# Optimization experiments

Measured on AMD Instinct MI355X. Metric: run time of the kernel, lower is better.

## Reference

```python
import jax, jax.numpy as jnp
import numpy as np

N = 50000          # nodes
E = 400000         # edges
MUL0 = 16          # multiplicity of 0e irreps (node & message)
MUL1 = 8           # multiplicity of 1o irreps
RBF = 8
HID = 64
CUTOFF = 5.0
WNUM = MUL0*MUL0 + MUL1*MUL0 + MUL0*MUL1 + MUL1*MUL1  # 576 tp weights per edge
EPS = 1e-8
INV_SQRT3 = 1.0 / np.sqrt(3.0).astype(np.float32)
A_PATH = 1.0 / np.sqrt(float(MUL0 + MUL1))  # e3nn path normalization (fan_in = 24 for both outputs)


def _split_sv(x):
    # x: [n, 40] -> scalars [n,16], vectors [n,8,3]
    return x[:, :MUL0], x[:, MUL0:].reshape(-1, MUL1, 3)


def _irrep_norm(x):
    # RMS-normalize each irrep block separately (IrrepNorm)
    s, v = _split_sv(x)
    s_rms = jnp.sqrt(jnp.mean(s * s, axis=-1, keepdims=True) + EPS)
    v_rms = jnp.sqrt(jnp.mean(jnp.sum(v * v, axis=-1), axis=-1, keepdims=True) + EPS)
    return jnp.concatenate([s / s_rms, (v / v_rms[:, :, None]).reshape(-1, MUL1 * 3)], axis=-1)


def setup_inputs() -> dict:
    key = jax.random.key(0)
    ks = jax.random.split(key, 20)
    inp = {
        'x': jax.random.normal(ks[0], (N, MUL0 + 3 * MUL1), jnp.float32),
        'edge_src': jax.random.randint(ks[1], (E,), 0, N, jnp.int32),
        'edge_dst': jax.random.randint(ks[2], (E,), 0, N, jnp.int32),
        'edge_sh': jax.random.normal(ks[3], (E, 4), jnp.float32),
        'edge_rbf': jax.random.uniform(ks[4], (E, RBF), jnp.float32),
        'edge_len': jax.random.uniform(ks[5], (E,), jnp.float32) * CUTOFF,
        # radial MLP producing per-edge TP weights
        'w_r1': jax.random.normal(ks[6], (RBF, HID), jnp.float32) / np.sqrt(RBF),
        'b_r1': jnp.zeros((HID,), jnp.float32),
        'w_r2': jax.random.normal(ks[7], (HID, WNUM), jnp.float32) / np.sqrt(HID),
        'b_r2': jnp.zeros((WNUM,), jnp.float32),
        # edge gate MLP
        'w_g1': jax.random.normal(ks[8], (RBF, HID), jnp.float32) / np.sqrt(RBF),
        'b_g1': jnp.zeros((HID,), jnp.float32),
        'w_g2': jax.random.normal(ks[9], (HID, 1), jnp.float32) / np.sqrt(HID),
        'b_g2': jnp.zeros((1,), jnp.float32),
        # msg_linear: 16x0e+8x1o -> (16x0e scalars + 8x0e gates) + 8x1o gated
        'Wm_s': jax.random.normal(ks[10], (MUL0, MUL0 + MUL1), jnp.float32),
        'Wm_v': jax.random.normal(ks[11], (MUL1, MUL1), jnp.float32),
        # update_linear and self_linear: 16x0e+8x1o -> 16x0e+8x1o
        'Wu_s': jax.random.normal(ks[12], (MUL0, MUL0), jnp.float32),
        'Wu_v': jax.random.normal(ks[13], (MUL1, MUL1), jnp.float32),
        'Ws_s': jax.random.normal(ks[14], (MUL0, MUL0), jnp.float32),
        'Ws_v': jax.random.normal(ks[15], (MUL1, MUL1), jnp.float32),
        'res_scale': jnp.asarray(0.1, jnp.float32),
    }
    return inp


def reference(x, edge_src, edge_dst, edge_sh, edge_rbf, edge_len,
              w_r1, b_r1, w_r2, b_r2, w_g1, b_g1, w_g2, b_g2,
              Wm_s, Wm_v, Wu_s, Wu_v, Ws_s, Ws_v, res_scale):
    x_norm = _irrep_norm(x)
    xs, xv = _split_sv(x_norm)

    # per-edge TP weights from radial MLP
    w = jax.nn.silu(edge_rbf @ w_r1 + b_r1) @ w_r2 + b_r2            # [E, 576]
    o = MUL0 * MUL0
    w1 = w[:, :o].reshape(-1, MUL0, MUL0)                            # 0e x 0e -> 0e
    w2 = w[:, o:o + MUL1 * MUL0].reshape(-1, MUL1, MUL0)             # 1o x 1o -> 0e
    o += MUL1 * MUL0
    w3 = w[:, o:o + MUL0 * MUL1].reshape(-1, MUL0, MUL1)             # 0e x 1o -> 1o
    o += MUL0 * MUL1
    w4 = w[:, o:].reshape(-1, MUL1, MUL1)                            # 1o x 0e -> 1o

    # gather per-edge source features
    s_e = xs[edge_src]                                               # [E,16]
    v_e = xv[edge_src]                                               # [E,8,3]
    sh0 = edge_sh[:, :1]                                             # [E,1]
    sh1 = edge_sh[:, 1:4]                                            # [E,3]

    # fully-connected tensor product (CG for l<=1, component norm, path norm)
    m0 = A_PATH * (jnp.einsum('ei,eij->ej', s_e * sh0, w1)
                   + INV_SQRT3 * jnp.einsum('eic,ec,eij->ej', v_e, sh1, w2))   # [E,16]
    m1 = A_PATH * (jnp.einsum('ei,eij,ec->ejc', s_e, w3, sh1)
                   + jnp.einsum('eic,eij->ejc', v_e * sh0[:, :, None], w4))    # [E,8,3]

    # cutoff and sigmoid edge gate
    cw = 0.5 * (jnp.cos(jnp.pi * edge_len / CUTOFF) + 1.0) * (edge_len < CUTOFF)
    gw = jax.nn.sigmoid(jax.nn.silu(edge_rbf @ w_g1 + b_g1) @ w_g2 + b_g2)     # [E,1]
    ew = cw[:, None] * gw                                                      # [E,1]
    m0 = m0 * ew
    m1 = m1 * ew[:, :, None]

    # scatter-add into destination nodes, normalize by total edge weight
    agg0 = jax.ops.segment_sum(m0, edge_dst, num_segments=N)                   # [N,16]
    agg1 = jax.ops.segment_sum(m1.reshape(-1, MUL1 * 3), edge_dst, num_segments=N).reshape(-1, MUL1, 3)
    norm = jax.ops.segment_sum(ew, edge_dst, num_segments=N)                   # [N,1]
    norm = jnp.maximum(norm, EPS)
    agg0 = agg0 / norm
    agg1 = agg1 / norm[:, :, None]

    # msg_linear (equivariant linear, fan-in normalized)
    sc = agg0 @ Wm_s / np.sqrt(MUL0)                                           # [N,24]
    vv = jnp.einsum('nic,ij->njc', agg1, Wm_v) / np.sqrt(MUL1)                 # [N,8,3]

    # gated nonlinearity
    scal = jax.nn.silu(sc[:, :MUL0])
    gates = jax.nn.sigmoid(sc[:, MUL0:])
    vg = vv * gates[:, :, None]

    # update + self interaction, residual
    out_s = scal @ Wu_s / np.sqrt(MUL0) + xs @ Ws_s / np.sqrt(MUL0)
    out_v = (jnp.einsum('nic,ij->njc', vg, Wu_v) + jnp.einsum('nic,ij->njc', xv, Ws_v)) / np.sqrt(MUL1)
    out = jnp.concatenate([out_s, out_v.reshape(-1, MUL1 * 3)], axis=-1)
    return x + res_scale * out
```

## Files before the change

kernel.cpp:

```cpp
#include <hip/hip_runtime.h>
#include <cstdint>

#define MUL0 16
#define MUL1 8
#define NRBF 8
#define HID 64
#define WNUM 576
#define CUTOFF 5.0f
#define EPSF 1e-8f

#define INV_SQRT3 0.57735026918962576f
#define A_PATH    0.20412414523193154f
#define Q16       0.25f
#define Q8        0.35355339059327373f
#define PI_OVER_CUT 0.62831853071795865f

typedef _Float16 f16;
typedef _Float16 f16x8 __attribute__((ext_vector_type(8)));
typedef float f32x4 __attribute__((ext_vector_type(4)));

#define MFMA16(a, b, cc) __builtin_amdgcn_mfma_f32_16x16x32_f16(a, b, cc, 0, 0, 0)

__device__ __forceinline__ float sigm(float x) { return 1.0f / (1.0f + __expf(-x)); }

typedef __attribute__((address_space(1))) const unsigned char* gptr_t;
typedef __attribute__((address_space(3))) unsigned char* lptr_t;

__device__ __forceinline__ void stage16(const void* g, void* l) {
  __builtin_amdgcn_global_load_lds((gptr_t)g, (lptr_t)l, 16, 0, 0);
}

extern "C" __global__ __launch_bounds__(256) void k_pre(
    const float* __restrict__ x, float* __restrict__ xnorm,
    float* __restrict__ agg0, float* __restrict__ agg1,
    float* __restrict__ normb, const float* __restrict__ w_r2,
    f16* __restrict__ W2T, int N) {
  int gid = blockIdx.x * 256 + threadIdx.x;

  if (gid < HID * WNUM) {
    int n = gid >> 6, k = gid & 63;
    int jt = n >> 4, cc = n & 15;
    int h = k >> 3, e = k & 7;
    int dst = jt * 1024 + cc * 64 + ((h ^ (cc & 7)) << 3) + e;
    W2T[dst] = (f16)w_r2[k * WNUM + n];
  }

  if (gid < N) {
    long long n = gid;
    const float4* xr = (const float4*)(x + n * 40);
    float4 vv[10];
#pragma unroll
    for (int i = 0; i < 10; i++) vv[i] = xr[i];
    float* f = (float*)vv;
    float ss = 0.f, vs = 0.f;
#pragma unroll
    for (int i = 0; i < 16; i++) ss += f[i] * f[i];
#pragma unroll
    for (int i = 16; i < 40; i++) vs += f[i] * f[i];
    float sr = rsqrtf(ss * (1.0f / 16.0f) + EPSF);
    float vr = rsqrtf(vs * (1.0f / 8.0f) + EPSF);
#pragma unroll
    for (int i = 0; i < 16; i++) f[i] *= sr;
#pragma unroll
    for (int i = 16; i < 40; i++) f[i] *= vr;
    float4* o = (float4*)(xnorm + n * 40);
#pragma unroll
    for (int i = 0; i < 10; i++) o[i] = vv[i];
    float4 z = {0.f, 0.f, 0.f, 0.f};
    float4* pa0 = (float4*)(agg0 + n * 16);
#pragma unroll
    for (int i = 0; i < 4; i++) pa0[i] = z;
    float4* pa1 = (float4*)(agg1 + n * 24);
#pragma unroll
    for (int i = 0; i < 6; i++) pa1[i] = z;
    normb[n] = 0.f;
  }
}

extern "C" __global__ __launch_bounds__(256, 3) void k_edge(
    const float* __restrict__ xnorm,
    const int* __restrict__ esrc, const int* __restrict__ edst,
    const float* __restrict__ sh, const float* __restrict__ rbf,
    const float* __restrict__ elen,
    const float* __restrict__ w_r1, const float* __restrict__ b_r1,
    const float* __restrict__ w_g1, const float* __restrict__ b_g1,
    const float* __restrict__ w_g2, const float* __restrict__ b_g2,
    const float* __restrict__ b_r2, const f16* __restrict__ W2T,
    float* __restrict__ agg0, float* __restrict__ agg1,
    float* __restrict__ normb, int E) {
  __shared__ __align__(16) char smem[53248];
  f16   (*s_H)[32][72]  = (f16(*)[32][72])(smem);
  float (*s_sn)[32][20] = (float(*)[32][20])(smem + 18432);
  float (*s_v)[32][26]  = (float(*)[32][26])(smem + 28672);
  float (*s_a1)[32][10] = (float(*)[32][10])(smem + 41984);
  float (*s_sh)[32][4]  = (float(*)[32][4])(smem + 47104);
  float (*s_rbf)[32][8] = (float(*)[32][8])(smem + 49152);
  float* s_bias = (float*)(smem + 49152);

  const int t = threadIdx.x;
  const int w = t >> 6;
  const int lane = t & 63;
  const long long eb = (long long)blockIdx.x * 128 + w * 32;

  int dstv = 0, srcv = 0;
  float lenv = 1e9f;
  if (lane < 32) {
    long long g2 = eb + lane;
    float4 shv = {0.f, 0.f, 0.f, 0.f};
    if (g2 < E) {
      srcv = esrc[g2];
      dstv = edst[g2];
      lenv = elen[g2];
      shv = *(const float4*)&sh[g2 * 4];
    }
    *(float4*)&s_sh[w][lane][0] = shv;
  }
  {
    int e = lane >> 1, half = lane & 1;
    long long ge2 = eb + e;
    float4 rv4 = {0.f, 0.f, 0.f, 0.f};
    if (ge2 < E) rv4 = *(const float4*)&rbf[ge2 * 8 + half * 4];
    *(float4*)&s_rbf[w][e][half * 4] = rv4;
  }
  __syncthreads();

  {
    const int ge_l = lane >> 2;
    const int part = lane & 3;
#pragma unroll
    for (int g = 0; g < 2; g++) {
      int e = g * 16 + ge_l;
      int srcn = __shfl(srcv, e);
      const float* xr = xnorm + (long long)srcn * 40;
      if (part < 2) {
        float4 aLo = *(const float4*)(xr + part * 8);
        float4 aHi = *(const float4*)(xr + part * 8 + 4);
        *(float4*)&s_sn[w][e][part * 8] = aLo;
        *(float4*)&s_sn[w][e][part * 8 + 4] = aHi;
      } else {
        const int i0 = (part - 2) * 4;
        const float* vp = xr + 16 + i0 * 3;
        float4 v0 = *(const float4*)(vp);
        float4 v1 = *(const float4*)(vp + 4);
        float4 v2 = *(const float4*)(vp + 8);
        *(float4*)&s_v[w][e][i0 * 3] = v0;
        *(float4*)&s_v[w][e][i0 * 3 + 4] = v1;
        *(float4*)&s_v[w][e][i0 * 3 + 8] = v2;
        float4 shq = *(const float4*)&s_sh[w][e][0];
        float s1x = shq.y, s1y = shq.z, s1z = shq.w;
        s_a1[w][e][i0]     = INV_SQRT3 * (v0.x * s1x + v0.y * s1y + v0.z * s1z);
        s_a1[w][e][i0 + 1] = INV_SQRT3 * (v0.w * s1x + v1.x * s1y + v1.y * s1z);
        s_a1[w][e][i0 + 2] = INV_SQRT3 * (v1.z * s1x + v1.w * s1y + v2.x * s1z);
        s_a1[w][e][i0 + 3] = INV_SQRT3 * (v2.y * s1x + v2.z * s1y + v2.w * s1z);
      }
    }
  }

  {
    float wr[8];
#pragma unroll
    for (int r = 0; r < 8; r++) wr[r] = w_r1[r * HID + lane];
    float bh = b_r1[lane];
#pragma unroll 4
    for (int u = 0; u < 32; u++) {
      float4 ra = *(const float4*)&s_rbf[w][u][0];
      float4 rb2 = *(const float4*)&s_rbf[w][u][4];
      float acc = bh + ra.x * wr[0] + ra.y * wr[1] + ra.z * wr[2] + ra.w * wr[3]
                     + rb2.x * wr[4] + rb2.y * wr[5] + rb2.z * wr[6] + rb2.w * wr[7];
      s_H[w][u][lane] = (f16)(acc * sigm(acc));
    }
  }

  float ewv = 0.f;
  {
    const int eg = lane & 31;
    const int hf = lane >> 5;
    float4 ga = *(const float4*)&s_rbf[w][eg][0];
    float4 gb = *(const float4*)&s_rbf[w][eg][4];
    float rv[8] = {ga.x, ga.y, ga.z, ga.w, gb.x, gb.y, gb.z, gb.w};
    float accp = 0.f;
#pragma unroll
    for (int ch = 0; ch < 2; ch++) {
      const int base = hf * 32 + ch * 16;
      float ttv[16];
      {
        const float4 b0 = *(const float4*)&b_g1[base];
        const float4 b1 = *(const float4*)&b_g1[base + 4];
        const float4 b2 = *(const float4*)&b_g1[base + 8];
        const float4 b3 = *(const float4*)&b_g1[base + 12];
        ttv[0] = b0.x; ttv[1] = b0.y; ttv[2] = b0.z; ttv[3] = b0.w;
        ttv[4] = b1.x; ttv[5] = b1.y; ttv[6] = b1.z; ttv[7] = b1.w;
        ttv[8] = b2.x; ttv[9] = b2.y; ttv[10] = b2.z; ttv[11] = b2.w;
        ttv[12] = b3.x; ttv[13] = b3.y; ttv[14] = b3.z; ttv[15] = b3.w;
      }
#pragma unroll
      for (int r = 0; r < 8; r++) {
        const float* wg = w_g1 + r * HID + base;
        float4 w0 = *(const float4*)(wg);
        float4 w1 = *(const float4*)(wg + 4);
        float4 w2 = *(const float4*)(wg + 8);
        float4 w3 = *(const float4*)(wg + 12);
        float rr = rv[r];
        ttv[0] += rr * w0.x; ttv[1] += rr * w0.y; ttv[2] += rr * w0.z; ttv[3] += rr * w0.w;
        ttv[4] += rr * w1.x; ttv[5] += rr * w1.y; ttv[6] += rr * w1.z; ttv[7] += rr * w1.w;
        ttv[8] += rr * w2.x; ttv[9] += rr * w2.y; ttv[10] += rr * w2.z; ttv[11] += rr * w2.w;
        ttv[12] += rr * w3.x; ttv[13] += rr * w3.y; ttv[14] += rr * w3.z; ttv[15] += rr * w3.w;
      }
      const float4 g0 = *(const float4*)&w_g2[base];
      const float4 g1 = *(const float4*)&w_g2[base + 4];
      const float4 g2 = *(const float4*)&w_g2[base + 8];
      const float4 g3 = *(const float4*)&w_g2[base + 12];
      float gw[16] = {g0.x, g0.y, g0.z, g0.w, g1.x, g1.y, g1.z, g1.w,
                      g2.x, g2.y, g2.z, g2.w, g3.x, g3.y, g3.z, g3.w};
#pragma unroll
      for (int k = 0; k < 16; k++) accp += ttv[k] * sigm(ttv[k]) * gw[k];
    }
    accp += __shfl_xor(accp, 32);
    if (lane < 32) {
      long long g2e = eb + lane;
      if (g2e < E) {
        float cw = (lenv < CUTOFF) ? 0.5f * (__cosf(PI_OVER_CUT * lenv) + 1.0f) : 0.f;
        ewv = cw * sigm(accp + b_g2[0]);
      }
    }
  }
  __syncthreads();

  const int quad = lane >> 4;
  const int c = lane & 15;

  const f16x8 af00 = *(const f16x8*)&s_H[w][c][quad * 8];
  const f16x8 af01 = *(const f16x8*)&s_H[w][c][32 + quad * 8];
  const f16x8 af10 = *(const f16x8*)&s_H[w][16 + c][quad * 8];
  const f16x8 af11 = *(const f16x8*)&s_H[w][16 + c][32 + quad * 8];
  for (int i = t; i < WNUM; i += 256) s_bias[i] = b_r2[i];
  __syncthreads();

  char* ring = smem;
  const char* W2Tc = (const char*)W2T;
  const int lofs = w * 1024;
  const int gofs = w * 1024 + lane * 16;

  stage16(W2Tc + gofs, ring + lofs);
  stage16(W2Tc + 4096 + gofs, ring + 4096 + lofs);

  const int rd0 = c * 128 + ((quad ^ (c & 7)) << 4);
  const int rd1 = c * 128 + (((quad + 4) ^ (c & 7)) << 4);

  float p1[2][4] = {{0.f}}, p2[2][4] = {{0.f}}, t3[2][4] = {{0.f}};
  float mx[2][4] = {{0.f}}, my[2][4] = {{0.f}}, mz[2][4] = {{0.f}};

#pragma unroll 1
  for (int ch = 0; ch < 4; ch++) {
    __syncthreads();
    stage16(W2Tc + (ch + 1) * 8192 + gofs, ring + ((ch + 1) & 1) * 8192 + lofs);
    stage16(W2Tc + (ch + 1) * 8192 + 4096 + gofs,
            ring + ((ch + 1) & 1) * 8192 + 4096 + lofs);
    const char* bb = ring + (ch & 1) * 8192;
#pragma unroll
    for (int q = 0; q < 4; q++) {
      const int jt = ch * 4 + q;
      const char* tb = bb + q * 2048;
      f16x8 b0 = *(const f16x8*)(tb + rd0);
      f16x8 b1 = *(const f16x8*)(tb + rd1);
      float bias = s_bias[jt * 16 + c];
      f32x4 C0 = {0.f, 0.f, 0.f, 0.f};
      C0 = MFMA16(af00, b0, C0); C0 = MFMA16(af01, b1, C0);
      f32x4 C1 = {0.f, 0.f, 0.f, 0.f};
      C1 = MFMA16(af10, b0, C1); C1 = MFMA16(af11, b1, C1);
#pragma unroll
      for (int r = 0; r < 4; r++) {
        p1[0][r] += s_sn[w][quad * 4 + r][jt] * (C0[r] + bias);
        p1[1][r] += s_sn[w][16 + quad * 4 + r][jt] * (C1[r] + bias);
      }
    }
  }
#pragma unroll 1
  for (int ch = 4; ch < 6; ch++) {
    __syncthreads();
    stage16(W2Tc + (ch + 1) * 8192 + gofs, ring + ((ch + 1) & 1) * 8192 + lofs);
    stage16(W2Tc + (ch + 1) * 8192 + 4096 + gofs,
            ring + ((ch + 1) & 1) * 8192 + 4096 + lofs);
    const char* bb = ring + (ch & 1) * 8192;
#pragma unroll
    for (int q = 0; q < 4; q++) {
      const int jt = ch * 4 + q;
      const char* tb = bb + q * 2048;
      f16x8 b0 = *(const f16x8*)(tb + rd0);
      f16x8 b1 = *(const f16x8*)(tb + rd1);
      float bias = s_bias[jt * 16 + c];
      f32x4 C0 = {0.f, 0.f, 0.f, 0.f};
      C0 = MFMA16(af00, b0, C0); C0 = MFMA16(af01, b1, C0);
      f32x4 C1 = {0.f, 0.f, 0.f, 0.f};
      C1 = MFMA16(af10, b0, C1); C1 = MFMA16(af11, b1, C1);
      const int i = jt - 16;
#pragma unroll
      for (int r = 0; r < 4; r++) {
        p2[0][r] += s_a1[w][quad * 4 + r][i] * (C0[r] + bias);
        p2[1][r] += s_a1[w][16 + quad * 4 + r][i] * (C1[r] + bias);
      }
    }
  }
#pragma unroll 1
  for (int ch = 6; ch < 8; ch++) {
    __syncthreads();
    stage16(W2Tc + (ch + 1) * 8192 + gofs, ring + ((ch + 1) & 1) * 8192 + lofs);
    stage16(W2Tc + (ch + 1) * 8192 + 4096 + gofs,
            ring + ((ch + 1) & 1) * 8192 + 4096 + lofs);
    const char* bb = ring + (ch & 1) * 8192;
#pragma unroll
    for (int q = 0; q < 4; q++) {
      const int jt = ch * 4 + q;
      const char* tb = bb + q * 2048;
      f16x8 b0 = *(const f16x8*)(tb + rd0);
      f16x8 b1 = *(const f16x8*)(tb + rd1);
      float bias = s_bias[jt * 16 + c];
      f32x4 C0 = {0.f, 0.f, 0.f, 0.f};
      C0 = MFMA16(af00, b0, C0); C0 = MFMA16(af01, b1, C0);
      f32x4 C1 = {0.f, 0.f, 0.f, 0.f};
      C1 = MFMA16(af10, b0, C1); C1 = MFMA16(af11, b1, C1);
      const int i = (jt - 24) * 2 + (c >> 3);
#pragma unroll
      for (int r = 0; r < 4; r++) {
        t3[0][r] += s_sn[w][quad * 4 + r][i] * (C0[r] + bias);
        t3[1][r] += s_sn[w][16 + quad * 4 + r][i] * (C1[r] + bias);
      }
    }
  }
  {
    __syncthreads();
    const char* bb = ring + (8 & 1) * 8192;
#pragma unroll
    for (int q = 0; q < 4; q++) {
      const int jt = 32 + q;
      const char* tb = bb + q * 2048;
      f16x8 b0 = *(const f16x8*)(tb + rd0);
      f16x8 b1 = *(const f16x8*)(tb + rd1);
      float bias = s_bias[jt * 16 + c];
      f32x4 C0 = {0.f, 0.f, 0.f, 0.f};
      C0 = MFMA16(af00, b0, C0); C0 = MFMA16(af01, b1, C0);
      f32x4 C1 = {0.f, 0.f, 0.f, 0.f};
      C1 = MFMA16(af10, b0, C1); C1 = MFMA16(af11, b1, C1);
      const int i = q * 2 + (c >> 3);
#pragma unroll
      for (int r = 0; r < 4; r++) {
        float wv0 = C0[r] + bias;
        float wv1 = C1[r] + bias;
        mx[0][r] += s_v[w][quad * 4 + r][3 * i] * wv0;
        my[0][r] += s_v[w][quad * 4 + r][3 * i + 1] * wv0;
        mz[0][r] += s_v[w][quad * 4 + r][3 * i + 2] * wv0;
        mx[1][r] += s_v[w][16 + quad * 4 + r][3 * i] * wv1;
        my[1][r] += s_v[w][16 + quad * 4 + r][3 * i + 1] * wv1;
        mz[1][r] += s_v[w][16 + quad * 4 + r][3 * i + 2] * wv1;
      }
    }
  }

#pragma unroll
  for (int g = 0; g < 2; g++)
#pragma unroll
    for (int r = 0; r < 4; r++) {
      t3[g][r] += __shfl_xor(t3[g][r], 8);
      mx[g][r] += __shfl_xor(mx[g][r], 8);
      my[g][r] += __shfl_xor(my[g][r], 8);
      mz[g][r] += __shfl_xor(mz[g][r], 8);
    }

#pragma unroll
  for (int g = 0; g < 2; g++) {
    const int e0g = g * 16 + quad * 4;
    int cur = __shfl(dstv, e0g);
    float acc0 = 0.f, a1x = 0.f, a1y = 0.f, a1z = 0.f, nacc = 0.f;
#pragma unroll
    for (int r = 0; r < 4; r++) {
      const int e = e0g + r;
      const int dst = __shfl(dstv, e);
      const float ew = __shfl(ewv, e);
      if (dst != cur) {
        atomicAdd(&agg0[(long long)cur * 16 + c], acc0);
        if (c < 8) {
          long long b = (long long)cur * 24 + (long long)c * 3;
          atomicAdd(&agg1[b], a1x);
          atomicAdd(&agg1[b + 1], a1y);
          atomicAdd(&agg1[b + 2], a1z);
        } else if (c == 8) {
          atomicAdd(&normb[cur], nacc);
        }
        acc0 = a1x = a1y = a1z = nacc = 0.f;
        cur = dst;
      }
      float sc2 = A_PATH * ew;
      float sh0 = s_sh[w][e][0];
      acc0 += (sh0 * p1[g][r] + p2[g][r]) * sc2;
      if (c < 8) {
        float t3v = t3[g][r] * sc2;
        float scs = sc2 * sh0;
        a1x += t3v * s_sh[w][e][1] + mx[g][r] * scs;
        a1y += t3v * s_sh[w][e][2] + my[g][r] * scs;
        a1z += t3v * s_sh[w][e][3] + mz[g][r] * scs;
      } else if (c == 8) {
        nacc += ew;
      }
    }
    atomicAdd(&agg0[(long long)cur * 16 + c], acc0);
    if (c < 8) {
      long long b = (long long)cur * 24 + (long long)c * 3;
      atomicAdd(&agg1[b], a1x);
      atomicAdd(&agg1[b + 1], a1y);
      atomicAdd(&agg1[b + 2], a1z);
    } else if (c == 8) {
      atomicAdd(&normb[cur], nacc);
    }
  }
}

extern "C" __global__ __launch_bounds__(64) void k_node(
    const float* __restrict__ x, const float* __restrict__ xnorm,
    const float* __restrict__ agg0, const float* __restrict__ agg1,
    const float* __restrict__ normb, const float* __restrict__ Wm_s,
    const float* __restrict__ Wm_v, const float* __restrict__ Wu_s,
    const float* __restrict__ Wu_v, const float* __restrict__ Ws_s,
    const float* __restrict__ Ws_v, const float* __restrict__ res_scale_p,
    float* __restrict__ out, int N) {
  __shared__ float sWms[384];
  __shared__ float sWmv[64];
  __shared__ float sWus[256];
  __shared__ float sWuv[64];
  __shared__ float sWss[256];
  __shared__ float sWsv[64];
  int t = threadIdx.x;
  for (int i = t; i < 384; i += 64) sWms[i] = Wm_s[i];
  sWmv[t] = Wm_v[t];
  for (int i = t; i < 256; i += 64) sWus[i] = Wu_s[i];
  sWuv[t] = Wu_v[t];
  for (int i = t; i < 256; i += 64) sWss[i] = Ws_s[i];
  sWsv[t] = Ws_v[t];
  __syncthreads();
  int n = blockIdx.x * 64 + t;
  if (n >= N) return;

  float inv = 1.0f / fmaxf(normb[n], EPSF);
  float4 a04[4], a14[6];
  {
    const float4* p = (const float4*)(agg0 + (long long)n * 16);
#pragma unroll
    for (int i = 0; i < 4; i++) a04[i] = p[i];
    const float4* q = (const float4*)(agg1 + (long long)n * 24);
#pragma unroll
    for (int i = 0; i < 6; i++) a14[i] = q[i];
  }
  float* a0 = (float*)a04;
  float* a1 = (float*)a14;
#pragma unroll
  for (int i = 0; i < 16; i++) a0[i] *= inv;
#pragma unroll
  for (int i = 0; i < 24; i++) a1[i] *= inv;

  float scal[16], gate[8];
#pragma unroll
  for (int jj = 0; jj < 24; jj++) {
    float acc = 0.f;
#pragma unroll
    for (int i = 0; i < 16; i++) acc += a0[i] * sWms[i * 24 + jj];
    acc *= Q16;
    if (jj < 16) scal[jj] = acc * sigm(acc);
    else gate[jj - 16] = sigm(acc);
  }
  float vg[24];
#pragma unroll
  for (int j = 0; j < 8; j++) {
    float g = gate[j];
#pragma unroll
    for (int cc = 0; cc < 3; cc++) {
      float acc = 0.f;
#pragma unroll
      for (int i = 0; i < 8; i++) acc += a1[i * 3 + cc] * sWmv[i * 8 + j];
      vg[j * 3 + cc] = acc * Q8 * g;
    }
  }
  float4 xn4[10], xo4[10];
  {
    const float4* p = (const float4*)(xnorm + (long long)n * 40);
    const float4* q = (const float4*)(x + (long long)n * 40);
#pragma unroll
    for (int i = 0; i < 10; i++) { xn4[i] = p[i]; xo4[i] = q[i]; }
  }
  const float* xn = (const float*)xn4;
  const float* xo = (const float*)xo4;
  float rs = res_scale_p[0];

  float4 ob[10];
  float* ov = (float*)ob;
#pragma unroll
  for (int j = 0; j < 16; j++) {
    float acc = 0.f, acc2 = 0.f;
#pragma unroll
    for (int i = 0; i < 16; i++) {
      acc += scal[i] * sWus[i * 16 + j];
      acc2 += xn[i] * sWss[i * 16 + j];
    }
    ov[j] = xo[j] + rs * ((acc + acc2) * Q16);
  }
#pragma unroll
  for (int j = 0; j < 8; j++) {
#pragma unroll
    for (int cc = 0; cc < 3; cc++) {
      float acc = 0.f;
#pragma unroll
      for (int i = 0; i < 8; i++)
        acc += vg[i * 3 + cc] * sWuv[i * 8 + j] + xn[16 + i * 3 + cc] * sWsv[i * 8 + j];
      ov[16 + j * 3 + cc] = xo[16 + j * 3 + cc] + rs * (acc * Q8);
    }
  }
  float4* po = (float4*)(out + (long long)n * 40);
#pragma unroll
  for (int i = 0; i < 10; i++) po[i] = ob[i];
}

extern "C" void kernel_launch(void* const* d_in, const int* in_sizes, int n_in,
                              void* d_out, int out_size, void* d_ws, size_t ws_size,
                              hipStream_t stream) {
  const float* x = (const float*)d_in[0];
  const int* esrc = (const int*)d_in[1];
  const int* edst = (const int*)d_in[2];
  const float* sh = (const float*)d_in[3];
  const float* rbf = (const float*)d_in[4];
  const float* elen = (const float*)d_in[5];
  const float* w_r1 = (const float*)d_in[6];
  const float* b_r1 = (const float*)d_in[7];
  const float* w_r2 = (const float*)d_in[8];
  const float* b_r2 = (const float*)d_in[9];
  const float* w_g1 = (const float*)d_in[10];
  const float* b_g1 = (const float*)d_in[11];
  const float* w_g2 = (const float*)d_in[12];
  const float* b_g2 = (const float*)d_in[13];
  const float* Wm_s = (const float*)d_in[14];
  const float* Wm_v = (const float*)d_in[15];
  const float* Wu_s = (const float*)d_in[16];
  const float* Wu_v = (const float*)d_in[17];
  const float* Ws_s = (const float*)d_in[18];
  const float* Ws_v = (const float*)d_in[19];
  const float* res_scale = (const float*)d_in[20];

  const int N = in_sizes[0] / 40;
  const int E = in_sizes[1];

  char* ws = (char*)d_ws;
  size_t off = 0;
  float* xnorm = (float*)(ws + off); off += (size_t)N * 40 * sizeof(float);
  off = (off + 255) & ~(size_t)255;
  float* agg0 = (float*)(ws + off); off += (size_t)N * 16 * sizeof(float);
  float* agg1 = (float*)(ws + off); off += (size_t)N * 24 * sizeof(float);
  float* normb = (float*)(ws + off); off += (size_t)N * sizeof(float);
  off = (off + 255) & ~(size_t)255;
  f16* W2T = (f16*)(ws + off); off += (size_t)WNUM * 64 * sizeof(f16);

  const int nbN = (N + 255) / 256;

  k_pre<<<nbN, 256, 0, stream>>>(x, xnorm, agg0, agg1, normb, w_r2, W2T, N);

  int nblk = (E + 127) / 128;
  k_edge<<<nblk, 256, 0, stream>>>(xnorm, esrc, edst, sh, rbf, elen,
                                   w_r1, b_r1, w_g1, b_g1, w_g2, b_g2, b_r2,
                                   W2T, agg0, agg1, normb, E);

  k_node<<<(N + 63) / 64, 64, 0, stream>>>(x, xnorm, agg0, agg1, normb, Wm_s,
                                           Wm_v, Wu_s, Wu_v, Ws_s, Ws_v,
                                           res_scale, (float*)d_out, N);
}
```

Measured before the change: 329.2 us.

## Make edge kernel persistent with full TP weight matrix resident in LDS

Turns k_edge into a persistent kernel: a grid capped at 640 blocks loops over edge tiles, and each block stages the whole f16 W2T matrix (72 KB) plus the bias into shared memory once. This replaces the per-tile double-buffered streaming of W2T from global memory and the barriers that went with it. The cost is about 126 KB of LDS per block, which drops occupancy to one block per CU (launch bounds changed to 1), so less latency hiding is available for the gathers and atomics.

```diff
diff --git a/kernel.cpp b/kernel.cpp
--- a/kernel.cpp
+++ b/kernel.cpp
@@ -77,7 +77,7 @@
   }
 }
 
-extern "C" __global__ __launch_bounds__(256, 3) void k_edge(
+extern "C" __global__ __launch_bounds__(256, 1) void k_edge(
     const float* __restrict__ xnorm,
     const int* __restrict__ esrc, const int* __restrict__ edst,
     const float* __restrict__ sh, const float* __restrict__ rbf,
@@ -87,180 +87,175 @@
     const float* __restrict__ w_g2, const float* __restrict__ b_g2,
     const float* __restrict__ b_r2, const f16* __restrict__ W2T,
     float* __restrict__ agg0, float* __restrict__ agg1,
-    float* __restrict__ normb, int E) {
-  __shared__ __align__(16) char smem[53248];
+    float* __restrict__ normb, int E, int ntiles) {
+  __shared__ __align__(16) char smem[129280];
   f16   (*s_H)[32][72]  = (f16(*)[32][72])(smem);
   float (*s_sn)[32][20] = (float(*)[32][20])(smem + 18432);
   float (*s_v)[32][26]  = (float(*)[32][26])(smem + 28672);
   float (*s_a1)[32][10] = (float(*)[32][10])(smem + 41984);
   float (*s_sh)[32][4]  = (float(*)[32][4])(smem + 47104);
   float (*s_rbf)[32][8] = (float(*)[32][8])(smem + 49152);
-  float* s_bias = (float*)(smem + 49152);
+  char*  wlds  = smem + 53248;
+  float* s_bias = (float*)(smem + 126976);
 
   const int t = threadIdx.x;
   const int w = t >> 6;
   const int lane = t & 63;
-  const long long eb = (long long)blockIdx.x * 128 + w * 32;
-
-  int dstv = 0, srcv = 0;
-  float lenv = 1e9f;
-  if (lane < 32) {
-    long long g2 = eb + lane;
-    float4 shv = {0.f, 0.f, 0.f, 0.f};
-    if (g2 < E) {
-      srcv = esrc[g2];
-      dstv = edst[g2];
-      lenv = elen[g2];
-      shv = *(const float4*)&sh[g2 * 4];
-    }
-    *(float4*)&s_sh[w][lane][0] = shv;
-  }
+
   {
-    int e = lane >> 1, half = lane & 1;
-    long long ge2 = eb + e;
-    float4 rv4 = {0.f, 0.f, 0.f, 0.f};
-    if (ge2 < E) rv4 = *(const float4*)&rbf[ge2 * 8 + half * 4];
-    *(float4*)&s_rbf[w][e][half * 4] = rv4;
-  }
-  __syncthreads();
-
-  {
-    const int ge_l = lane >> 2;
-    const int part = lane & 3;
-#pragma unroll
-    for (int g = 0; g < 2; g++) {
-      int e = g * 16 + ge_l;
-      int srcn = __shfl(srcv, e);
-      const float* xr = xnorm + (long long)srcn * 40;
-      if (part < 2) {
-        float4 aLo = *(const float4*)(xr + part * 8);
-        float4 aHi = *(const float4*)(xr + part * 8 + 4);
-        *(float4*)&s_sn[w][e][part * 8] = aLo;
-        *(float4*)&s_sn[w][e][part * 8 + 4] = aHi;
-      } else {
-        const int i0 = (part - 2) * 4;
-        const float* vp = xr + 16 + i0 * 3;
-        float4 v0 = *(const float4*)(vp);
-        float4 v1 = *(const float4*)(vp + 4);
-        float4 v2 = *(const float4*)(vp + 8);
-        *(float4*)&s_v[w][e][i0 * 3] = v0;
-        *(float4*)&s_v[w][e][i0 * 3 + 4] = v1;
-        *(float4*)&s_v[w][e][i0 * 3 + 8] = v2;
-        float4 shq = *(const float4*)&s_sh[w][e][0];
-        float s1x = shq.y, s1y = shq.z, s1z = shq.w;
-        s_a1[w][e][i0]     = INV_SQRT3 * (v0.x * s1x + v0.y * s1y + v0.z * s1z);
-        s_a1[w][e][i0 + 1] = INV_SQRT3 * (v0.w * s1x + v1.x * s1y + v1.y * s1z);
-        s_a1[w][e][i0 + 2] = INV_SQRT3 * (v1.z * s1x + v1.w * s1y + v2.x * s1z);
-        s_a1[w][e][i0 + 3] = INV_SQRT3 * (v2.y * s1x + v2.z * s1y + v2.w * s1z);
-      }
-    }
-  }
-
-  {
-    float wr[8];
-#pragma unroll
-    for (int r = 0; r < 8; r++) wr[r] = w_r1[r * HID + lane];
-    float bh = b_r1[lane];
-#pragma unroll 4
-    for (int u = 0; u < 32; u++) {
-      float4 ra = *(const float4*)&s_rbf[w][u][0];
-      float4 rb2 = *(const float4*)&s_rbf[w][u][4];
-      float acc = bh + ra.x * wr[0] + ra.y * wr[1] + ra.z * wr[2] + ra.w * wr[3]
-                     + rb2.x * wr[4] + rb2.y * wr[5] + rb2.z * wr[6] + rb2.w * wr[7];
-      s_H[w][u][lane] = (f16)(acc * sigm(acc));
-    }
-  }
-
-  float ewv = 0.f;
-  {
-    const int eg = lane & 31;
-    const int hf = lane >> 5;
-    float4 ga = *(const float4*)&s_rbf[w][eg][0];
-    float4 gb = *(const float4*)&s_rbf[w][eg][4];
-    float rv[8] = {ga.x, ga.y, ga.z, ga.w, gb.x, gb.y, gb.z, gb.w};
-    float accp = 0.f;
-#pragma unroll
-    for (int ch = 0; ch < 2; ch++) {
-      const int base = hf * 32 + ch * 16;
-      float ttv[16];
-      {
-        const float4 b0 = *(const float4*)&b_g1[base];
-        const float4 b1 = *(const float4*)&b_g1[base + 4];
-        const float4 b2 = *(const float4*)&b_g1[base + 8];
-        const float4 b3 = *(const float4*)&b_g1[base + 12];
-        ttv[0] = b0.x; ttv[1] = b0.y; ttv[2] = b0.z; ttv[3] = b0.w;
-        ttv[4] = b1.x; ttv[5] = b1.y; ttv[6] = b1.z; ttv[7] = b1.w;
-        ttv[8] = b2.x; ttv[9] = b2.y; ttv[10] = b2.z; ttv[11] = b2.w;
-        ttv[12] = b3.x; ttv[13] = b3.y; ttv[14] = b3.z; ttv[15] = b3.w;
-      }
-#pragma unroll
-      for (int r = 0; r < 8; r++) {
-        const float* wg = w_g1 + r * HID + base;
-        float4 w0 = *(const float4*)(wg);
-        float4 w1 = *(const float4*)(wg + 4);
-        float4 w2 = *(const float4*)(wg + 8);
-        float4 w3 = *(const float4*)(wg + 12);
-        float rr = rv[r];
-        ttv[0] += rr * w0.x; ttv[1] += rr * w0.y; ttv[2] += rr * w0.z; ttv[3] += rr * w0.w;
-        ttv[4] += rr * w1.x; ttv[5] += rr * w1.y; ttv[6] += rr * w1.z; ttv[7] += rr * w1.w;
-        ttv[8] += rr * w2.x; ttv[9] += rr * w2.y; ttv[10] += rr * w2.z; ttv[11] += rr * w2.w;
-        ttv[12] += rr * w3.x; ttv[13] += rr * w3.y; ttv[14] += rr * w3.z; ttv[15] += rr * w3.w;
-      }
-      const float4 g0 = *(const float4*)&w_g2[base];
-      const float4 g1 = *(const float4*)&w_g2[base + 4];
-      const float4 g2 = *(const float4*)&w_g2[base + 8];
-      const float4 g3 = *(const float4*)&w_g2[base + 12];
-      float gw[16] = {g0.x, g0.y, g0.z, g0.w, g1.x, g1.y, g1.z, g1.w,
-                      g2.x, g2.y, g2.z, g2.w, g3.x, g3.y, g3.z, g3.w};
-#pragma unroll
-      for (int k = 0; k < 16; k++) accp += ttv[k] * sigm(ttv[k]) * gw[k];
-    }
-    accp += __shfl_xor(accp, 32);
-    if (lane < 32) {
-      long long g2e = eb + lane;
-      if (g2e < E) {
-        float cw = (lenv < CUTOFF) ? 0.5f * (__cosf(PI_OVER_CUT * lenv) + 1.0f) : 0.f;
-        ewv = cw * sigm(accp + b_g2[0]);
-      }
-    }
-  }
-  __syncthreads();
+    const char* W2Tc = (const char*)W2T;
+#pragma unroll 1
+    for (int k = 0; k < 18; k++)
+      stage16(W2Tc + k * 4096 + w * 1024 + lane * 16,
+              wlds + k * 4096 + w * 1024);
+    for (int i = t; i < WNUM; i += 256) s_bias[i] = b_r2[i];
+  }
 
   const int quad = lane >> 4;
   const int c = lane & 15;
-
-  const f16x8 af00 = *(const f16x8*)&s_H[w][c][quad * 8];
-  const f16x8 af01 = *(const f16x8*)&s_H[w][c][32 + quad * 8];
-  const f16x8 af10 = *(const f16x8*)&s_H[w][16 + c][quad * 8];
-  const f16x8 af11 = *(const f16x8*)&s_H[w][16 + c][32 + quad * 8];
-  for (int i = t; i < WNUM; i += 256) s_bias[i] = b_r2[i];
-  __syncthreads();
-
-  char* ring = smem;
-  const char* W2Tc = (const char*)W2T;
-  const int lofs = w * 1024;
-  const int gofs = w * 1024 + lane * 16;
-
-  stage16(W2Tc + gofs, ring + lofs);
-  stage16(W2Tc + 4096 + gofs, ring + 4096 + lofs);
-
   const int rd0 = c * 128 + ((quad ^ (c & 7)) << 4);
   const int rd1 = c * 128 + (((quad + 4) ^ (c & 7)) << 4);
 
-  float p1[2][4] = {{0.f}}, p2[2][4] = {{0.f}}, t3[2][4] = {{0.f}};
-  float mx[2][4] = {{0.f}}, my[2][4] = {{0.f}}, mz[2][4] = {{0.f}};
-
 #pragma unroll 1
-  for (int ch = 0; ch < 4; ch++) {
+  for (int vb = blockIdx.x; vb < ntiles; vb += gridDim.x) {
     __syncthreads();
-    stage16(W2Tc + (ch + 1) * 8192 + gofs, ring + ((ch + 1) & 1) * 8192 + lofs);
-    stage16(W2Tc + (ch + 1) * 8192 + 4096 + gofs,
-            ring + ((ch + 1) & 1) * 8192 + 4096 + lofs);
-    const char* bb = ring + (ch & 1) * 8192;
-#pragma unroll
-    for (int q = 0; q < 4; q++) {
-      const int jt = ch * 4 + q;
-      const char* tb = bb + q * 2048;
+    const long long eb = (long long)vb * 128 + w * 32;
+
+    int dstv = 0, srcv = 0;
+    float lenv = 1e9f;
+    if (lane < 32) {
+      long long g2 = eb + lane;
+      float4 shv = {0.f, 0.f, 0.f, 0.f};
+      if (g2 < E) {
+        srcv = esrc[g2];
+        dstv = edst[g2];
+        lenv = elen[g2];
+        shv = *(const float4*)&sh[g2 * 4];
+      }
+      *(float4*)&s_sh[w][lane][0] = shv;
+    }
+    {
+      int e = lane >> 1, half = lane & 1;
+      long long ge2 = eb + e;
+      float4 rv4 = {0.f, 0.f, 0.f, 0.f};
+      if (ge2 < E) rv4 = *(const float4*)&rbf[ge2 * 8 + half * 4];
+      *(float4*)&s_rbf[w][e][half * 4] = rv4;
+    }
+    __syncthreads();
+
+    {
+      const int ge_l = lane >> 2;
+      const int part = lane & 3;
+#pragma unroll
+      for (int g = 0; g < 2; g++) {
+        int e = g * 16 + ge_l;
+        int srcn = __shfl(srcv, e);
+        const float* xr = xnorm + (long long)srcn * 40;
+        if (part < 2) {
+          float4 aLo = *(const float4*)(xr + part * 8);
+          float4 aHi = *(const float4*)(xr + part * 8 + 4);
+          *(float4*)&s_sn[w][e][part * 8] = aLo;
+          *(float4*)&s_sn[w][e][part * 8 + 4] = aHi;
+        } else {
+          const int i0 = (part - 2) * 4;
+          const float* vp = xr + 16 + i0 * 3;
+          float4 v0 = *(const float4*)(vp);
+          float4 v1 = *(const float4*)(vp + 4);
+          float4 v2 = *(const float4*)(vp + 8);
+          *(float4*)&s_v[w][e][i0 * 3] = v0;
+          *(float4*)&s_v[w][e][i0 * 3 + 4] = v1;
+          *(float4*)&s_v[w][e][i0 * 3 + 8] = v2;
+          float4 shq = *(const float4*)&s_sh[w][e][0];
+          float s1x = shq.y, s1y = shq.z, s1z = shq.w;
+          s_a1[w][e][i0]     = INV_SQRT3 * (v0.x * s1x + v0.y * s1y + v0.z * s1z);
+          s_a1[w][e][i0 + 1] = INV_SQRT3 * (v0.w * s1x + v1.x * s1y + v1.y * s1z);
+          s_a1[w][e][i0 + 2] = INV_SQRT3 * (v1.z * s1x + v1.w * s1y + v2.x * s1z);
+          s_a1[w][e][i0 + 3] = INV_SQRT3 * (v2.y * s1x + v2.z * s1y + v2.w * s1z);
+        }
+      }
+    }
+
+    {
+      float wr[8];
+#pragma unroll
+      for (int r = 0; r < 8; r++) wr[r] = w_r1[r * HID + lane];
+      float bh = b_r1[lane];
+#pragma unroll 4
+      for (int u = 0; u < 32; u++) {
+        float4 ra = *(const float4*)&s_rbf[w][u][0];
+        float4 rb2 = *(const float4*)&s_rbf[w][u][4];
+        float acc = bh + ra.x * wr[0] + ra.y * wr[1] + ra.z * wr[2] + ra.w * wr[3]
+                       + rb2.x * wr[4] + rb2.y * wr[5] + rb2.z * wr[6] + rb2.w * wr[7];
+        s_H[w][u][lane] = (f16)(acc * sigm(acc));
+      }
+    }
+
+    float ewv = 0.f;
+    {
+      const int eg = lane & 31;
+      const int hf = lane >> 5;
+      float4 ga = *(const float4*)&s_rbf[w][eg][0];
+      float4 gb = *(const float4*)&s_rbf[w][eg][4];
+      float rv[8] = {ga.x, ga.y, ga.z, ga.w, gb.x, gb.y, gb.z, gb.w};
+      float accp = 0.f;
+#pragma unroll
+      for (int ch = 0; ch < 2; ch++) {
+        const int base = hf * 32 + ch * 16;
+        float ttv[16];
+        {
+          const float4 b0 = *(const float4*)&b_g1[base];
+          const float4 b1 = *(const float4*)&b_g1[base + 4];
+          const float4 b2 = *(const float4*)&b_g1[base + 8];
+          const float4 b3 = *(const float4*)&b_g1[base + 12];
+          ttv[0] = b0.x; ttv[1] = b0.y; ttv[2] = b0.z; ttv[3] = b0.w;
+          ttv[4] = b1.x; ttv[5] = b1.y; ttv[6] = b1.z; ttv[7] = b1.w;
+          ttv[8] = b2.x; ttv[9] = b2.y; ttv[10] = b2.z; ttv[11] = b2.w;
+          ttv[12] = b3.x; ttv[13] = b3.y; ttv[14] = b3.z; ttv[15] = b3.w;
+        }
+#pragma unroll
+        for (int r = 0; r < 8; r++) {
+          const float* wg = w_g1 + r * HID + base;
+          float4 w0 = *(const float4*)(wg);
+          float4 w1 = *(const float4*)(wg + 4);
+          float4 w2 = *(const float4*)(wg + 8);
+          float4 w3 = *(const float4*)(wg + 12);
+          float rr = rv[r];
+          ttv[0] += rr * w0.x; ttv[1] += rr * w0.y; ttv[2] += rr * w0.z; ttv[3] += rr * w0.w;
+          ttv[4] += rr * w1.x; ttv[5] += rr * w1.y; ttv[6] += rr * w1.z; ttv[7] += rr * w1.w;
+          ttv[8] += rr * w2.x; ttv[9] += rr * w2.y; ttv[10] += rr * w2.z; ttv[11] += rr * w2.w;
+          ttv[12] += rr * w3.x; ttv[13] += rr * w3.y; ttv[14] += rr * w3.z; ttv[15] += rr * w3.w;
+        }
+        const float4 g0 = *(const float4*)&w_g2[base];
+        const float4 g1 = *(const float4*)&w_g2[base + 4];
+        const float4 g2 = *(const float4*)&w_g2[base + 8];
+        const float4 g3 = *(const float4*)&w_g2[base + 12];
+        float gw[16] = {g0.x, g0.y, g0.z, g0.w, g1.x, g1.y, g1.z, g1.w,
+                        g2.x, g2.y, g2.z, g2.w, g3.x, g3.y, g3.z, g3.w};
+#pragma unroll
+        for (int k = 0; k < 16; k++) accp += ttv[k] * sigm(ttv[k]) * gw[k];
+      }
+      accp += __shfl_xor(accp, 32);
+      if (lane < 32) {
+        long long g2e = eb + lane;
+        if (g2e < E) {
+          float cw = (lenv < CUTOFF) ? 0.5f * (__cosf(PI_OVER_CUT * lenv) + 1.0f) : 0.f;
+          ewv = cw * sigm(accp + b_g2[0]);
+        }
+      }
+    }
+    __syncthreads();
+
+    const f16x8 af00 = *(const f16x8*)&s_H[w][c][quad * 8];
+    const f16x8 af01 = *(const f16x8*)&s_H[w][c][32 + quad * 8];
+    const f16x8 af10 = *(const f16x8*)&s_H[w][16 + c][quad * 8];
+    const f16x8 af11 = *(const f16x8*)&s_H[w][16 + c][32 + quad * 8];
+
+    float p1[2][4] = {{0.f}}, p2[2][4] = {{0.f}}, t3[2][4] = {{0.f}};
+    float mx[2][4] = {{0.f}}, my[2][4] = {{0.f}}, mz[2][4] = {{0.f}};
+
+#pragma unroll 2
+    for (int jt = 0; jt < 16; jt++) {
+      const char* tb = wlds + jt * 2048;
       f16x8 b0 = *(const f16x8*)(tb + rd0);
       f16x8 b1 = *(const f16x8*)(tb + rd1);
       float bias = s_bias[jt * 16 + c];
@@ -274,18 +269,9 @@
         p1[1][r] += s_sn[w][16 + quad * 4 + r][jt] * (C1[r] + bias);
       }
     }
-  }
-#pragma unroll 1
-  for (int ch = 4; ch < 6; ch++) {
-    __syncthreads();
-    stage16(W2Tc + (ch + 1) * 8192 + gofs, ring + ((ch + 1) & 1) * 8192 + lofs);
-    stage16(W2Tc + (ch + 1) * 8192 + 4096 + gofs,
-            ring + ((ch + 1) & 1) * 8192 + 4096 + lofs);
-    const char* bb = ring + (ch & 1) * 8192;
-#pragma unroll
-    for (int q = 0; q < 4; q++) {
-      const int jt = ch * 4 + q;
-      const char* tb = bb + q * 2048;
+#pragma unroll 2
+    for (int jt = 16; jt < 24; jt++) {
+      const char* tb = wlds + jt * 2048;
       f16x8 b0 = *(const f16x8*)(tb + rd0);
       f16x8 b1 = *(const f16x8*)(tb + rd1);
       float bias = s_bias[jt * 16 + c];
@@ -300,18 +286,9 @@
         p2[1][r] += s_a1[w][16 + quad * 4 + r][i] * (C1[r] + bias);
       }
     }
-  }
-#pragma unroll 1
-  for (int ch = 6; ch < 8; ch++) {
-    __syncthreads();
-    stage16(W2Tc + (ch + 1) * 8192 + gofs, ring + ((ch + 1) & 1) * 8192 + lofs);
-    stage16(W2Tc + (ch + 1) * 8192 + 4096 + gofs,
-            ring + ((ch + 1) & 1) * 8192 + 4096 + lofs);
-    const char* bb = ring + (ch & 1) * 8192;
-#pragma unroll
-    for (int q = 0; q < 4; q++) {
-      const int jt = ch * 4 + q;
-      const char* tb = bb + q * 2048;
+#pragma unroll 2
+    for (int jt = 24; jt < 32; jt++) {
+      const char* tb = wlds + jt * 2048;
       f16x8 b0 = *(const f16x8*)(tb + rd0);
       f16x8 b1 = *(const f16x8*)(tb + rd1);
       float bias = s_bias[jt * 16 + c];
@@ -326,14 +303,9 @@
         t3[1][r] += s_sn[w][16 + quad * 4 + r][i] * (C1[r] + bias);
       }
     }
-  }
-  {
-    __syncthreads();
-    const char* bb = ring + (8 & 1) * 8192;
-#pragma unroll
-    for (int q = 0; q < 4; q++) {
-      const int jt = 32 + q;
-      const char* tb = bb + q * 2048;
+#pragma unroll 2
+    for (int jt = 32; jt < 36; jt++) {
+      const char* tb = wlds + jt * 2048;
       f16x8 b0 = *(const f16x8*)(tb + rd0);
       f16x8 b1 = *(const f16x8*)(tb + rd1);
       float bias = s_bias[jt * 16 + c];
@@ -341,7 +313,7 @@
       C0 = MFMA16(af00, b0, C0); C0 = MFMA16(af01, b1, C0);
       f32x4 C1 = {0.f, 0.f, 0.f, 0.f};
       C1 = MFMA16(af10, b0, C1); C1 = MFMA16(af11, b1, C1);
-      const int i = q * 2 + (c >> 3);
+      const int i = (jt - 32) * 2 + (c >> 3);
 #pragma unroll
       for (int r = 0; r < 4; r++) {
         float wv0 = C0[r] + bias;
@@ -354,62 +326,62 @@
         mz[1][r] += s_v[w][16 + quad * 4 + r][3 * i + 2] * wv1;
       }
     }
-  }
-
-#pragma unroll
-  for (int g = 0; g < 2; g++)
-#pragma unroll
-    for (int r = 0; r < 4; r++) {
-      t3[g][r] += __shfl_xor(t3[g][r], 8);
-      mx[g][r] += __shfl_xor(mx[g][r], 8);
-      my[g][r] += __shfl_xor(my[g][r], 8);
-      mz[g][r] += __shfl_xor(mz[g][r], 8);
-    }
-
-#pragma unroll
-  for (int g = 0; g < 2; g++) {
-    const int e0g = g * 16 + quad * 4;
-    int cur = __shfl(dstv, e0g);
-    float acc0 = 0.f, a1x = 0.f, a1y = 0.f, a1z = 0.f, nacc = 0.f;
-#pragma unroll
-    for (int r = 0; r < 4; r++) {
-      const int e = e0g + r;
-      const int dst = __shfl(dstv, e);
-      const float ew = __shfl(ewv, e);
-      if (dst != cur) {
-        atomicAdd(&agg0[(long long)cur * 16 + c], acc0);
+
+#pragma unroll
+    for (int g = 0; g < 2; g++)
+#pragma unroll
+      for (int r = 0; r < 4; r++) {
+        t3[g][r] += __shfl_xor(t3[g][r], 8);
+        mx[g][r] += __shfl_xor(mx[g][r], 8);
+        my[g][r] += __shfl_xor(my[g][r], 8);
+        mz[g][r] += __shfl_xor(mz[g][r], 8);
+      }
+
+#pragma unroll
+    for (int g = 0; g < 2; g++) {
+      const int e0g = g * 16 + quad * 4;
+      int cur = __shfl(dstv, e0g);
+      float acc0 = 0.f, a1x = 0.f, a1y = 0.f, a1z = 0.f, nacc = 0.f;
+#pragma unroll
+      for (int r = 0; r < 4; r++) {
+        const int e = e0g + r;
+        const int dst = __shfl(dstv, e);
+        const float ew = __shfl(ewv, e);
+        if (dst != cur) {
+          atomicAdd(&agg0[(long long)cur * 16 + c], acc0);
+          if (c < 8) {
+            long long b = (long long)cur * 24 + (long long)c * 3;
+            atomicAdd(&agg1[b], a1x);
+            atomicAdd(&agg1[b + 1], a1y);
+            atomicAdd(&agg1[b + 2], a1z);
+          } else if (c == 8) {
+            atomicAdd(&normb[cur], nacc);
+          }
+          acc0 = a1x = a1y = a1z = nacc = 0.f;
+          cur = dst;
+        }
+        float sc2 = A_PATH * ew;
+        float sh0 = s_sh[w][e][0];
+        acc0 += (sh0 * p1[g][r] + p2[g][r]) * sc2;
         if (c < 8) {
-          long long b = (long long)cur * 24 + (long long)c * 3;
-          atomicAdd(&agg1[b], a1x);
-          atomicAdd(&agg1[b + 1], a1y);
-          atomicAdd(&agg1[b + 2], a1z);
+          float t3v = t3[g][r] * sc2;
+          float scs = sc2 * sh0;
+          a1x += t3v * s_sh[w][e][1] + mx[g][r] * scs;
+          a1y += t3v * s_sh[w][e][2] + my[g][r] * scs;
+          a1z += t3v * s_sh[w][e][3] + mz[g][r] * scs;
         } else if (c == 8) {
-          atomicAdd(&normb[cur], nacc);
+          nacc += ew;
         }
-        acc0 = a1x = a1y = a1z = nacc = 0.f;
-        cur = dst;
-      }
-      float sc2 = A_PATH * ew;
-      float sh0 = s_sh[w][e][0];
-      acc0 += (sh0 * p1[g][r] + p2[g][r]) * sc2;
+      }
+      atomicAdd(&agg0[(long long)cur * 16 + c], acc0);
       if (c < 8) {
-        float t3v = t3[g][r] * sc2;
-        float scs = sc2 * sh0;
-        a1x += t3v * s_sh[w][e][1] + mx[g][r] * scs;
-        a1y += t3v * s_sh[w][e][2] + my[g][r] * scs;
-        a1z += t3v * s_sh[w][e][3] + mz[g][r] * scs;
+        long long b = (long long)cur * 24 + (long long)c * 3;
+        atomicAdd(&agg1[b], a1x);
+        atomicAdd(&agg1[b + 1], a1y);
+        atomicAdd(&agg1[b + 2], a1z);
       } else if (c == 8) {
-        nacc += ew;
-      }
-    }
-    atomicAdd(&agg0[(long long)cur * 16 + c], acc0);
-    if (c < 8) {
-      long long b = (long long)cur * 24 + (long long)c * 3;
-      atomicAdd(&agg1[b], a1x);
-      atomicAdd(&agg1[b + 1], a1y);
-      atomicAdd(&agg1[b + 2], a1z);
-    } else if (c == 8) {
-      atomicAdd(&normb[cur], nacc);
+        atomicAdd(&normb[cur], nacc);
+      }
     }
   }
 }
@@ -559,10 +531,11 @@
 
   k_pre<<<nbN, 256, 0, stream>>>(x, xnorm, agg0, agg1, normb, w_r2, W2T, N);
 
-  int nblk = (E + 127) / 128;
-  k_edge<<<nblk, 256, 0, stream>>>(xnorm, esrc, edst, sh, rbf, elen,
-                                   w_r1, b_r1, w_g1, b_g1, w_g2, b_g2, b_r2,
-                                   W2T, agg0, agg1, normb, E);
+  int ntiles = (E + 127) / 128;
+  int gridE = ntiles < 640 ? ntiles : 640;
+  k_edge<<<gridE, 256, 0, stream>>>(xnorm, esrc, edst, sh, rbf, elen,
+                                    w_r1, b_r1, w_g1, b_g1, w_g2, b_g2, b_r2,
+                                    W2T, agg0, agg1, normb, E, ntiles);
 
   k_node<<<(N + 63) / 64, 64, 0, stream>>>(x, xnorm, agg0, agg1, normb, Wm_s,
                                            Wm_v, Wu_s, Wu_v, Ws_s, Ws_v,
```

Result: slower. 449.6 us (+36.6%).
